# Performance work log

Hardware: AMD Instinct MI355X
Metric: run time of the kernel (lower is better)

Reference implementation:

```python
import jax, jax.numpy as jnp
from jax import lax
import numpy as np

B, T, H, W, C = 16, 64, 64, 64, 3
ACTION_DIM = 2
ENC_FEAT = 2 * 2 * 256  # conv output 2x2x256 flattened
LSTM1, LSTM2 = 512, 256
FORGET_BIAS = 1.0


def setup_inputs() -> dict:
    key = jax.random.key(0)
    ks = jax.random.split(key, 20)
    f32 = jnp.float32

    def glorot(k, shape):
        fan_in = int(np.prod(shape[:-1]))
        return jax.random.normal(k, shape, f32) * np.sqrt(2.0 / fan_in)

    inp = {
        'frames': jax.random.normal(ks[0], (B, T, H, W, C), f32),
        'actions': jax.random.normal(ks[1], (B, T, ACTION_DIM), f32),
        # conv encoder: kernel 4, stride 2, VALID, relu
        'w1': glorot(ks[2], (4, 4, 3, 32)),   'b1': jnp.zeros((32,), f32),
        'w2': glorot(ks[3], (4, 4, 32, 64)),  'b2': jnp.zeros((64,), f32),
        'w3': glorot(ks[4], (4, 4, 64, 128)), 'b3': jnp.zeros((128,), f32),
        'w4': glorot(ks[5], (4, 4, 128, 256)),'b4': jnp.zeros((256,), f32),
        # LSTM cells, TF gate order (i, j, f, o)
        'k_l1': glorot(ks[6], (ENC_FEAT + ACTION_DIM + LSTM1, 4 * LSTM1)),
        'b_l1': jnp.zeros((4 * LSTM1,), f32),
        'k_l2': glorot(ks[7], (LSTM1 + LSTM2, 4 * LSTM2)),
        'b_l2': jnp.zeros((4 * LSTM2,), f32),
        # dense head
        'w_d1': glorot(ks[8], (LSTM2, 128)), 'b_d1': jnp.zeros((128,), f32),
        'w_d2': glorot(ks[9], (128, 1)),     'b_d2': jnp.zeros((1,), f32),
    }
    return inp


def _conv(x, w, b):
    y = lax.conv_general_dilated(x, w, (2, 2), 'VALID',
                                 dimension_numbers=('NHWC', 'HWIO', 'NHWC'))
    return jax.nn.relu(y + b)


def _lstm_cell(x, h, c, k, b, hidden):
    gates = jnp.concatenate([x, h], axis=-1) @ k + b
    i, j, f, o = jnp.split(gates, 4, axis=-1)
    c_new = jax.nn.sigmoid(f + FORGET_BIAS) * c + jax.nn.sigmoid(i) * jnp.tanh(j)
    h_new = jax.nn.sigmoid(o) * jnp.tanh(c_new)
    return h_new, c_new


def reference(frames, actions, w1, b1, w2, b2, w3, b3, w4, b4,
              k_l1, b_l1, k_l2, b_l2, w_d1, b_d1, w_d2, b_d2):
    b, t = frames.shape[0], frames.shape[1]
    # CNN encoder over all frames at once
    x = frames.reshape(b * t, H, W, C)
    x = _conv(x, w1, b1)
    x = _conv(x, w2, b2)
    x = _conv(x, w3, b3)
    x = _conv(x, w4, b4)                      # [b*t, 2, 2, 256]
    enc = x.reshape(b, t, ENC_FEAT)
    lstm_in = jnp.concatenate([enc, actions], axis=-1)  # [b, t, 1026]

    # 2-layer stacked LSTM via scan over time (time-major)
    xs = jnp.swapaxes(lstm_in, 0, 1)          # [t, b, 1026]
    c1 = jnp.zeros((b, LSTM1), frames.dtype)
    h1 = jnp.zeros((b, LSTM1), frames.dtype)
    c2 = jnp.zeros((b, LSTM2), frames.dtype)
    h2 = jnp.zeros((b, LSTM2), frames.dtype)

    def step(carry, x_t):
        c1, h1, c2, h2 = carry
        h1n, c1n = _lstm_cell(x_t, h1, c1, k_l1, b_l1, LSTM1)
        h2n, c2n = _lstm_cell(h1n, h2, c2, k_l2, b_l2, LSTM2)
        return (c1n, h1n, c2n, h2n), h2n

    _, hs = lax.scan(step, (c1, h1, c2, h2), xs)  # hs: [t, b, 256]
    lstm_out = jnp.swapaxes(hs, 0, 1)              # [b, t, 256]

    d1 = jax.nn.relu(lstm_out @ w_d1 + b_d1)
    out = d1 @ w_d2 + b_d2                          # [b, t, 1]
    return out
```

## Files before the change

### kernel.cpp

```cpp
#include <hip/hip_runtime.h>

#define DI __device__ __forceinline__

DI float sigm(float x)  { return 1.0f / (1.0f + __expf(-x)); }
DI float tanh_(float x) { return 2.0f / (1.0f + __expf(-2.0f * x)) - 1.0f; }

DI float cload(const float* p) {
  return __hip_atomic_load(p, __ATOMIC_RELAXED, __HIP_MEMORY_SCOPE_AGENT);
}
DI void cstore(float* p, float v) {
  __hip_atomic_store(p, v, __ATOMIC_RELAXED, __HIP_MEMORY_SCOPE_AGENT);
}

DI void fma4(float4& a, float s, const float4& w) {
  a.x += s * w.x; a.y += s * w.y; a.z += s * w.z; a.w += s * w.w;
}
DI float4 relu4(float4 a) {
  return make_float4(fmaxf(a.x, 0.f), fmaxf(a.y, 0.f), fmaxf(a.z, 0.f), fmaxf(a.w, 0.f));
}

__global__ void conv1_k4(const float* __restrict__ in, const float* __restrict__ w,
                         const float* __restrict__ bias, float* __restrict__ out) {
  int idx = blockIdx.x * 256 + threadIdx.x;
  if (idx >= 1024 * 31 * 16 * 8) return;
  int c4 = idx & 7;  int t = idx >> 3;
  int xp = t & 15;   t >>= 4;
  int y = t % 31;    int n = t / 31;
  const float* ip = in + (((size_t)n * 64 + 2 * y) * 64 + 4 * xp) * 3;
  bool v1 = (xp < 15);
  int off1 = v1 ? 6 : 0;
  float4 bv = *(const float4*)(bias + c4 * 4);
  float4 a0 = bv, a1 = bv;
#pragma unroll
  for (int ky = 0; ky < 4; ++ky) {
#pragma unroll
    for (int kx = 0; kx < 4; ++kx) {
      const float* ipr = ip + (ky * 64 + kx) * 3;
      const float* wp  = w + ((ky * 4 + kx) * 3) * 32 + c4 * 4;
#pragma unroll
      for (int ci = 0; ci < 3; ++ci) {
        float4 wv = *(const float4*)(wp + ci * 32);
        float i0 = ipr[ci], i1 = ipr[off1 + ci];
        fma4(a0, i0, wv);
        fma4(a1, i1, wv);
      }
    }
  }
  int x0 = 2 * xp;
  float* op = out + ((size_t)n * 31 * 31 + (size_t)y * 31 + x0) * 32 + c4 * 4;
  *(float4*)op = relu4(a0);
  if (v1) *(float4*)(op + 32) = relu4(a1);
}

template <int CIN, int COUT, int NTILE, int WIN, int WOUT>
__global__ __launch_bounds__(512)
void conv_lds2(const float* __restrict__ in, const float* __restrict__ w,
               const float* __restrict__ bias, float* __restrict__ out, int ostride) {
  constexpr int K    = 16 * CIN;
  constexpr int NC4  = NTILE / 4;
  constexpr int XPB  = 512 / NC4;
  constexpr int XPI  = (WOUT / 2) * WOUT;
  constexpr int XPH  = 1024 * XPI / 2;
  __shared__ float Wl[K * NTILE];
  const int tid = threadIdx.x;
  const int cs  = blockIdx.y;
  constexpr int TOT4 = K * NC4;
  for (int i = tid; i < TOT4; i += 512) {
    int k = i / NC4, c4 = i % NC4;
    *(float4*)&Wl[k * NTILE + c4 * 4] =
        *(const float4*)&w[(size_t)k * COUT + cs * NTILE + c4 * 4];
  }
  __syncthreads();
  const int c4l  = tid % NC4;
  const int xpul = tid / NC4;
  int g0 = blockIdx.x * XPB + xpul;
  int g1 = g0 + XPH;
  int n0 = g0 / XPI, r0 = g0 % XPI;
  int y0 = r0 / (WOUT / 2), xp0 = r0 % (WOUT / 2);
  int n1 = g1 / XPI, r1 = g1 % XPI;
  int y1 = r1 / (WOUT / 2), xp1 = r1 % (WOUT / 2);
  const float* ip0 = in + (((size_t)n0 * WIN + 2 * y0) * WIN + 4 * xp0) * CIN;
  const float* ip1 = in + (((size_t)n1 * WIN + 2 * y1) * WIN + 4 * xp1) * CIN;
  float4 bv = *(const float4*)(bias + cs * NTILE + c4l * 4);
  float4 a00 = bv, a01 = bv, a10 = bv, a11 = bv;
#pragma unroll
  for (int kk = 0; kk < 16; ++kk) {
    int ky = kk >> 2, kx = kk & 3;
    const float* i0r = ip0 + (ky * WIN + kx) * CIN;
    const float* i1r = ip1 + (ky * WIN + kx) * CIN;
    const float* wpr = Wl + kk * CIN * NTILE + c4l * 4;
#pragma unroll 4
    for (int ci4 = 0; ci4 < CIN / 4; ++ci4) {
      float4 p00 = *(const float4*)(i0r + ci4 * 4);
      float4 p01 = *(const float4*)(i0r + 2 * CIN + ci4 * 4);
      float4 p10 = *(const float4*)(i1r + ci4 * 4);
      float4 p11 = *(const float4*)(i1r + 2 * CIN + ci4 * 4);
      const float* wq = wpr + (size_t)(ci4 * 4) * NTILE;
      float4 w0 = *(const float4*)(wq);
      fma4(a00, p00.x, w0); fma4(a01, p01.x, w0); fma4(a10, p10.x, w0); fma4(a11, p11.x, w0);
      float4 w1v = *(const float4*)(wq + NTILE);
      fma4(a00, p00.y, w1v); fma4(a01, p01.y, w1v); fma4(a10, p10.y, w1v); fma4(a11, p11.y, w1v);
      float4 w2v = *(const float4*)(wq + 2 * NTILE);
      fma4(a00, p00.z, w2v); fma4(a01, p01.z, w2v); fma4(a10, p10.z, w2v); fma4(a11, p11.z, w2v);
      float4 w3v = *(const float4*)(wq + 3 * NTILE);
      fma4(a00, p00.w, w3v); fma4(a01, p01.w, w3v); fma4(a10, p10.w, w3v); fma4(a11, p11.w, w3v);
    }
  }
  float* o0 = out + (size_t)n0 * ostride + ((size_t)y0 * WOUT + 2 * xp0) * COUT + cs * NTILE + c4l * 4;
  *(float4*)o0          = relu4(a00);
  *(float4*)(o0 + COUT) = relu4(a01);
  float* o1 = out + (size_t)n1 * ostride + ((size_t)y1 * WOUT + 2 * xp1) * COUT + cs * NTILE + c4l * 4;
  *(float4*)o1          = relu4(a10);
  *(float4*)(o1 + COUT) = relu4(a11);
}

__global__ void act_copy(const float* __restrict__ act, float* __restrict__ xin) {
  int i = blockIdx.x * 256 + threadIdx.x;
  if (i < 2048) xin[(size_t)(i >> 1) * 1026 + 1024 + (i & 1)] = act[i];
}

__global__ void gemm_xpart(const float* __restrict__ A, const float* __restrict__ Bw,
                           const float* __restrict__ bias, float* __restrict__ C) {
  __shared__ float As[16][64];
  __shared__ float Bs[16][64];
  const int tid = threadIdx.x;
  const int tx = tid & 15, ty = tid >> 4;
  const int m0 = blockIdx.y * 64, n0 = blockIdx.x * 64;
  float acc[4][4] = {};
  for (int k0 = 0; k0 < 1026; k0 += 16) {
#pragma unroll
    for (int i = 0; i < 4; ++i) {
      int lin = tid + i * 256;
      int ka = lin & 15, mm = lin >> 4;
      As[ka][mm] = (k0 + ka < 1026) ? A[(size_t)(m0 + mm) * 1026 + k0 + ka] : 0.0f;
      int kb = lin >> 6, nn = lin & 63;
      Bs[kb][nn] = (k0 + kb < 1026) ? Bw[(size_t)(k0 + kb) * 2048 + n0 + nn] : 0.0f;
    }
    __syncthreads();
#pragma unroll
    for (int kk = 0; kk < 16; ++kk) {
      float av[4], bv[4];
#pragma unroll
      for (int i = 0; i < 4; ++i) { av[i] = As[kk][ty * 4 + i]; bv[i] = Bs[kk][tx * 4 + i]; }
#pragma unroll
      for (int i = 0; i < 4; ++i)
#pragma unroll
        for (int j = 0; j < 4; ++j) acc[i][j] += av[i] * bv[j];
    }
    __syncthreads();
  }
#pragma unroll
  for (int i = 0; i < 4; ++i) {
    int m = m0 + ty * 4 + i;
    int xrow = (m & 63) * 16 + (m >> 6);
#pragma unroll
    for (int j = 0; j < 4; ++j) {
      int n = n0 + tx * 4 + j;
      C[(size_t)xrow * 2048 + n] = acc[i][j] + bias[n];
    }
  }
}

__global__ void __launch_bounds__(512, 1)
lstm_k(const float* __restrict__ xpart,
       const float* __restrict__ kl1,
       const float* __restrict__ kl2,
       const float* __restrict__ bl2,
       float* __restrict__ h1b, float* __restrict__ c1,
       float* __restrict__ h2b, float* __restrict__ c2,
       unsigned* __restrict__ bar,
       float* __restrict__ out_seq) {
  __shared__ float big[12544];
  __shared__ float red2[2176];
  __shared__ float gs1[544];
  __shared__ float gs2[272];
  float* stg1 = big;
  float* red1 = big + 8192;
  float* stg2 = big;
  const int tid = threadIdx.x;
  const int blk = blockIdx.x;
  const float* Wh1 = kl1 + (size_t)1026 * 2048;

  const int cA  = tid & 31, ks1 = tid >> 5;
  const int k0A = ks1 * 32;
  const int pA  = (cA & 3) * 512 + blk * 8 + (cA >> 2);
  const int cB  = tid & 15, ks2 = tid >> 4;
  const int k0B = ks2 * 24;
  const int pB  = (cB & 3) * 256 + blk * 4 + (cB >> 2);
  const int cR  = tid >> 4, bR = tid & 15;
  const int pR1 = (cR & 3) * 512 + blk * 8 + (cR >> 2);
  const int pR2 = (cR & 3) * 256 + blk * 4 + (cR >> 2);

  float w1r[32], w2r[24];
#pragma unroll
  for (int i = 0; i < 32; ++i) w1r[i] = Wh1[(size_t)(k0A + i) * 2048 + pA];
#pragma unroll
  for (int i = 0; i < 24; ++i) w2r[i] = kl2[(size_t)(k0B + i) * 1024 + pB];
  const float blv = bl2[pR2];

  for (int t = 0; t < 64; ++t) {
    const float* h1c = h1b + (size_t)(t & 1) * 8192;
    float* h1n       = h1b + (size_t)((t + 1) & 1) * 8192;
    const float* h2c = h2b + (size_t)(t & 1) * 4096;
    float* h2n       = h2b + (size_t)((t + 1) & 1) * 4096;

    float xpv = xpart[(size_t)((t << 4) + bR) * 2048 + pR1];

    float sv[16];
#pragma unroll
    for (int j = 0; j < 16; ++j) sv[j] = cload(h1c + (j << 9) + tid);
    __syncthreads();
#pragma unroll
    for (int j = 0; j < 16; ++j) stg1[(j << 9) + tid] = sv[j];
    __syncthreads();

    float acc[16];
#pragma unroll
    for (int b = 0; b < 16; ++b) acc[b] = 0.f;
#pragma unroll
    for (int bp = 0; bp < 8; ++bp) {
      const float* pa = stg1 + (bp * 2) * 512 + k0A;
      const float* pb = pa + 512;
      float4 va[8], vb[8];
#pragma unroll
      for (int i = 0; i < 8; ++i) va[i] = *(const float4*)(pa + i * 4);
#pragma unroll
      for (int i = 0; i < 8; ++i) vb[i] = *(const float4*)(pb + i * 4);
      const float* fa = (const float*)va;
      const float* fb = (const float*)vb;
#pragma unroll
      for (int j = 0; j < 32; ++j) {
        acc[bp * 2]     = fmaf(w1r[j], fa[j], acc[bp * 2]);
        acc[bp * 2 + 1] = fmaf(w1r[j], fb[j], acc[bp * 2 + 1]);
      }
    }
    {
      float fc[16];
#pragma unroll
      for (int b = 0; b < 16; ++b) fc[b] = acc[b] + __shfl_xor(acc[b], 32);
      int p = tid >> 6;
      int half = (ks1 & 1) * 8;
      float* dst = red1 + p * 544 + cA * 17 + half;
#pragma unroll
      for (int j = 0; j < 8; ++j) dst[j] = fc[half + j];
    }
    __syncthreads();
    {
      float s = xpv;
#pragma unroll
      for (int p = 0; p < 8; ++p) s += red1[p * 544 + cR * 17 + bR];
      gs1[cR * 17 + bR] = s;
    }
    __syncthreads();
    if (tid < 128) {
      int u_l = tid >> 4, b = tid & 15;
      int u = blk * 8 + u_l;
      float gi = gs1[(u_l * 4 + 0) * 17 + b];
      float gj = gs1[(u_l * 4 + 1) * 17 + b];
      float gf = gs1[(u_l * 4 + 2) * 17 + b];
      float go = gs1[(u_l * 4 + 3) * 17 + b];
      float cold = c1[b * 512 + u];
      float cn = sigm(gf + 1.0f) * cold + sigm(gi) * tanh_(gj);
      float hn = sigm(go) * tanh_(cn);
      c1[b * 512 + u] = cn;
      cstore(h1n + b * 512 + u, hn);
    }
    __syncthreads();

    if (tid == 0) {
      unsigned tgt = 8u * (t + 1);
      unsigned old = __hip_atomic_fetch_add(&bar[(blk >> 3) * 32], 1u,
                                            __ATOMIC_RELAXED, __HIP_MEMORY_SCOPE_AGENT);
      if (old == tgt - 1)
        __hip_atomic_fetch_add(&bar[256], 1u, __ATOMIC_RELAXED, __HIP_MEMORY_SCOPE_AGENT);
      while (__hip_atomic_load(&bar[256], __ATOMIC_RELAXED, __HIP_MEMORY_SCOPE_AGENT) < tgt)
        __builtin_amdgcn_s_sleep(2);
    }
    __syncthreads();

    float sw[24];
#pragma unroll
    for (int j = 0; j < 24; ++j) {
      int e = (j << 9) + tid;
      sw[j] = (j < 16) ? cload(h1n + e) : cload(h2c + (e - 8192));
    }
#pragma unroll
    for (int j = 0; j < 24; ++j) {
      if (j < 16) stg2[j * 768 + tid] = sw[j];
      else {
        int b = (j - 16) * 2 + (tid >> 8);
        stg2[b * 768 + 512 + (tid & 255)] = sw[j];
      }
    }
    __syncthreads();

#pragma unroll
    for (int b = 0; b < 16; ++b) acc[b] = 0.f;
#pragma unroll
    for (int bp = 0; bp < 8; ++bp) {
      const float* pa = stg2 + (bp * 2) * 768 + k0B;
      const float* pb = pa + 768;
      float4 va[6], vb[6];
#pragma unroll
      for (int i = 0; i < 6; ++i) va[i] = *(const float4*)(pa + i * 4);
#pragma unroll
      for (int i = 0; i < 6; ++i) vb[i] = *(const float4*)(pb + i * 4);
      const float* fa = (const float*)va;
      const float* fb = (const float*)vb;
#pragma unroll
      for (int j = 0; j < 24; ++j) {
        acc[bp * 2]     = fmaf(w2r[j], fa[j], acc[bp * 2]);
        acc[bp * 2 + 1] = fmaf(w2r[j], fb[j], acc[bp * 2 + 1]);
      }
    }
    {
      float fc[16];
#pragma unroll
      for (int b = 0; b < 16; ++b) {
        float s = acc[b] + __shfl_xor(acc[b], 16);
        fc[b] = s + __shfl_xor(s, 32);
      }
      int q = tid >> 6;
      int s4 = (ks2 & 3) * 4;
      float* dst = red2 + q * 272 + cB * 17 + s4;
#pragma unroll
      for (int j = 0; j < 4; ++j) dst[j] = fc[s4 + j];
    }
    __syncthreads();
    if (tid < 256) {
      float s = blv;
#pragma unroll
      for (int p = 0; p < 8; ++p) s += red2[p * 272 + cR * 17 + bR];
      gs2[cR * 17 + bR] = s;
    }
    __syncthreads();
    if (tid < 64) {
      int u_l = tid >> 4, b = tid & 15;
      int u = blk * 4 + u_l;
      float gi = gs2[(u_l * 4 + 0) * 17 + b];
      float gj = gs2[(u_l * 4 + 1) * 17 + b];
      float gf = gs2[(u_l * 4 + 2) * 17 + b];
      float go = gs2[(u_l * 4 + 3) * 17 + b];
      float cold = c2[b * 256 + u];
      float cn = sigm(gf + 1.0f) * cold + sigm(gi) * tanh_(gj);
      float hn = sigm(go) * tanh_(cn);
      c2[b * 256 + u] = cn;
      cstore(h2n + b * 256 + u, hn);
      out_seq[(size_t)((b << 6) + t) * 256 + u] = hn;
    }
  }
}

__global__ void head_k(const float* __restrict__ xin, const float* __restrict__ wd1,
                       const float* __restrict__ bd1, const float* __restrict__ wd2,
                       const float* __restrict__ bd2, float* __restrict__ out) {
  __shared__ float xs[4][256];
  __shared__ float ps[4][128];
  int r0 = blockIdx.x * 4;
  int tid = threadIdx.x;
  for (int i = tid; i < 1024; i += 128) xs[i >> 8][i & 255] = xin[(size_t)r0 * 256 + i];
  __syncthreads();
  float w2 = wd2[tid];
  float bb = bd1[tid];
#pragma unroll
  for (int rr = 0; rr < 4; ++rr) {
    float acc = bb;
#pragma unroll 8
    for (int k = 0; k < 256; ++k) acc += xs[rr][k] * wd1[k * 128 + tid];
    ps[rr][tid] = fmaxf(acc, 0.0f) * w2;
  }
  __syncthreads();
  if (tid < 4) {
    float s = bd2[0];
    for (int k = 0; k < 128; ++k) s += ps[tid][k];
    out[r0 + tid] = s;
  }
}

extern "C" void kernel_launch(void* const* d_in, const int* in_sizes, int n_in,
                              void* d_out, int out_size, void* d_ws, size_t ws_size,
                              hipStream_t stream) {
  const float* frames  = (const float*)d_in[0];
  const float* actions = (const float*)d_in[1];
  const float* w1 = (const float*)d_in[2];   const float* b1 = (const float*)d_in[3];
  const float* w2 = (const float*)d_in[4];   const float* b2 = (const float*)d_in[5];
  const float* w3 = (const float*)d_in[6];   const float* b3 = (const float*)d_in[7];
  const float* w4 = (const float*)d_in[8];   const float* b4 = (const float*)d_in[9];
  const float* kl1 = (const float*)d_in[10]; const float* bl1 = (const float*)d_in[11];
  const float* kl2 = (const float*)d_in[12]; const float* bl2 = (const float*)d_in[13];
  const float* wd1 = (const float*)d_in[14]; const float* bd1 = (const float*)d_in[15];
  const float* wd2 = (const float*)d_in[16]; const float* bd2 = (const float*)d_in[17];
  float* out = (float*)d_out;

  float* ws = (float*)d_ws;
  float* a1    = ws;
  float* a2    = ws + 31490048u;
  float* a3    = ws;
  float* xin   = ws + 31490048u;
  float* xpart = ws + 44335104u;
  float* h1b   = ws + 46432256u;
  float* c1    = ws + 46448640u;
  float* h2b   = ws + 46456832u;
  float* c2    = ws + 46465024u;
  unsigned* bar = (unsigned*)(ws + 46469120u);
  float* lout  = ws + 46469632u;

  hipMemsetAsync(h1b, 0, (36864 + 512) * sizeof(float), stream);

  conv1_k4<<<15872, 256, 0, stream>>>(frames, w1, b1, a1);
  conv_lds2<32, 64, 32, 31, 14><<<dim3(784, 2), 512, 0, stream>>>(a1, w2, b2, a2, 14 * 14 * 64);
  conv_lds2<64, 128, 16, 14, 6><<<dim3(72, 8), 512, 0, stream>>>(a2, w3, b3, a3, 6 * 6 * 128);
  conv_lds2<128, 256, 8, 6, 2><<<dim3(4, 32), 512, 0, stream>>>(a3, w4, b4, xin, 1026);
  act_copy<<<8, 256, 0, stream>>>(actions, xin);
  gemm_xpart<<<dim3(32, 16), 256, 0, stream>>>(xin, kl1, bl1, xpart);

  void* args[10];
  args[0] = (void*)&xpart; args[1] = (void*)&kl1; args[2] = (void*)&kl2; args[3] = (void*)&bl2;
  args[4] = (void*)&h1b;   args[5] = (void*)&c1;  args[6] = (void*)&h2b; args[7] = (void*)&c2;
  args[8] = (void*)&bar;   args[9] = (void*)&lout;
  hipLaunchCooperativeKernel((void*)lstm_k, dim3(64), dim3(512), args, 0, stream);

  head_k<<<256, 128, 0, stream>>>(lout, wd1, bd1, wd2, bd2, out);
}
```

Before: 2.773 ms.

## Split LSTM layers into pipelined block groups with per-block flags; restructure conv loop

The cooperative LSTM kernel now runs layer 1 on 64 blocks and layer 2 on 16 separate blocks. The two groups synchronise through per-block step flags instead of one global barrier, so layer 2 of step t can overlap layer 1 of step t+1. The conv kernels drop from four output pairs per thread to two, with a software-prefetched row of inputs reused across kx, and launch twice as many blocks. This adds polling traffic and heavier register use in layer-2 blocks (96 weights each), in exchange for shorter serial dependency chains and better conv load scheduling.

```diff
diff --git a/kernel.cpp b/kernel.cpp
--- a/kernel.cpp
+++ b/kernel.cpp
@@ -9,6 +9,12 @@
   return __hip_atomic_load(p, __ATOMIC_RELAXED, __HIP_MEMORY_SCOPE_AGENT);
 }
 DI void cstore(float* p, float v) {
+  __hip_atomic_store(p, v, __ATOMIC_RELAXED, __HIP_MEMORY_SCOPE_AGENT);
+}
+DI unsigned uload(const unsigned* p) {
+  return __hip_atomic_load(p, __ATOMIC_RELAXED, __HIP_MEMORY_SCOPE_AGENT);
+}
+DI void ustore(unsigned* p, unsigned v) {
   __hip_atomic_store(p, v, __ATOMIC_RELAXED, __HIP_MEMORY_SCOPE_AGENT);
 }
 
@@ -54,13 +60,14 @@
 
 template <int CIN, int COUT, int NTILE, int WIN, int WOUT>
 __global__ __launch_bounds__(512)
-void conv_lds2(const float* __restrict__ in, const float* __restrict__ w,
+void conv_lds3(const float* __restrict__ in, const float* __restrict__ w,
                const float* __restrict__ bias, float* __restrict__ out, int ostride) {
   constexpr int K    = 16 * CIN;
   constexpr int NC4  = NTILE / 4;
   constexpr int XPB  = 512 / NC4;
   constexpr int XPI  = (WOUT / 2) * WOUT;
-  constexpr int XPH  = 1024 * XPI / 2;
+  constexpr int C4N  = CIN / 4;
+  constexpr int NIT  = 4 * C4N;
   __shared__ float Wl[K * NTILE];
   const int tid = threadIdx.x;
   const int cs  = blockIdx.y;
@@ -73,45 +80,44 @@
   __syncthreads();
   const int c4l  = tid % NC4;
   const int xpul = tid / NC4;
-  int g0 = blockIdx.x * XPB + xpul;
-  int g1 = g0 + XPH;
-  int n0 = g0 / XPI, r0 = g0 % XPI;
-  int y0 = r0 / (WOUT / 2), xp0 = r0 % (WOUT / 2);
-  int n1 = g1 / XPI, r1 = g1 % XPI;
-  int y1 = r1 / (WOUT / 2), xp1 = r1 % (WOUT / 2);
-  const float* ip0 = in + (((size_t)n0 * WIN + 2 * y0) * WIN + 4 * xp0) * CIN;
-  const float* ip1 = in + (((size_t)n1 * WIN + 2 * y1) * WIN + 4 * xp1) * CIN;
+  int gxp = blockIdx.x * XPB + xpul;
+  int n = gxp / XPI, r = gxp % XPI;
+  int y = r / (WOUT / 2), xp = r % (WOUT / 2);
+  const float* ip = in + (((size_t)n * WIN + 2 * y) * WIN + 4 * xp) * CIN;
   float4 bv = *(const float4*)(bias + cs * NTILE + c4l * 4);
-  float4 a00 = bv, a01 = bv, a10 = bv, a11 = bv;
-#pragma unroll
-  for (int kk = 0; kk < 16; ++kk) {
-    int ky = kk >> 2, kx = kk & 3;
-    const float* i0r = ip0 + (ky * WIN + kx) * CIN;
-    const float* i1r = ip1 + (ky * WIN + kx) * CIN;
-    const float* wpr = Wl + kk * CIN * NTILE + c4l * 4;
-#pragma unroll 4
-    for (int ci4 = 0; ci4 < CIN / 4; ++ci4) {
-      float4 p00 = *(const float4*)(i0r + ci4 * 4);
-      float4 p01 = *(const float4*)(i0r + 2 * CIN + ci4 * 4);
-      float4 p10 = *(const float4*)(i1r + ci4 * 4);
-      float4 p11 = *(const float4*)(i1r + 2 * CIN + ci4 * 4);
-      const float* wq = wpr + (size_t)(ci4 * 4) * NTILE;
+  float4 a0 = bv, a1 = bv;
+
+  float4 cur[6], nxt[6];
+#pragma unroll
+  for (int cc = 0; cc < 6; ++cc) cur[cc] = *(const float4*)(ip + cc * CIN);
+#pragma unroll 2
+  for (int it = 0; it < NIT; ++it) {
+    int ky = it / C4N, ci4 = it % C4N;
+    if (it + 1 < NIT) {
+      int ky2 = (it + 1) / C4N, ci42 = (it + 1) % C4N;
+      const float* base = ip + (ky2 * WIN) * CIN + ci42 * 4;
+#pragma unroll
+      for (int cc = 0; cc < 6; ++cc) nxt[cc] = *(const float4*)(base + cc * CIN);
+    }
+    const float* wr = Wl + ((ky * 4) * CIN + ci4 * 4) * NTILE + c4l * 4;
+#pragma unroll
+    for (int kx = 0; kx < 4; ++kx) {
+      const float* wq = wr + (size_t)kx * CIN * NTILE;
       float4 w0 = *(const float4*)(wq);
-      fma4(a00, p00.x, w0); fma4(a01, p01.x, w0); fma4(a10, p10.x, w0); fma4(a11, p11.x, w0);
+      fma4(a0, cur[kx].x, w0);     fma4(a1, cur[kx + 2].x, w0);
       float4 w1v = *(const float4*)(wq + NTILE);
-      fma4(a00, p00.y, w1v); fma4(a01, p01.y, w1v); fma4(a10, p10.y, w1v); fma4(a11, p11.y, w1v);
+      fma4(a0, cur[kx].y, w1v);    fma4(a1, cur[kx + 2].y, w1v);
       float4 w2v = *(const float4*)(wq + 2 * NTILE);
-      fma4(a00, p00.z, w2v); fma4(a01, p01.z, w2v); fma4(a10, p10.z, w2v); fma4(a11, p11.z, w2v);
+      fma4(a0, cur[kx].z, w2v);    fma4(a1, cur[kx + 2].z, w2v);
       float4 w3v = *(const float4*)(wq + 3 * NTILE);
-      fma4(a00, p00.w, w3v); fma4(a01, p01.w, w3v); fma4(a10, p10.w, w3v); fma4(a11, p11.w, w3v);
-    }
-  }
-  float* o0 = out + (size_t)n0 * ostride + ((size_t)y0 * WOUT + 2 * xp0) * COUT + cs * NTILE + c4l * 4;
-  *(float4*)o0          = relu4(a00);
-  *(float4*)(o0 + COUT) = relu4(a01);
-  float* o1 = out + (size_t)n1 * ostride + ((size_t)y1 * WOUT + 2 * xp1) * COUT + cs * NTILE + c4l * 4;
-  *(float4*)o1          = relu4(a10);
-  *(float4*)(o1 + COUT) = relu4(a11);
+      fma4(a0, cur[kx].w, w3v);    fma4(a1, cur[kx + 2].w, w3v);
+    }
+#pragma unroll
+    for (int cc = 0; cc < 6; ++cc) cur[cc] = nxt[cc];
+  }
+  float* op = out + (size_t)n * ostride + ((size_t)y * WOUT + 2 * xp) * COUT + cs * NTILE + c4l * 4;
+  *(float4*)op          = relu4(a0);
+  *(float4*)(op + COUT) = relu4(a1);
 }
 
 __global__ void act_copy(const float* __restrict__ act, float* __restrict__ xin) {
@@ -168,185 +174,198 @@
        const float* __restrict__ bl2,
        float* __restrict__ h1b, float* __restrict__ c1,
        float* __restrict__ h2b, float* __restrict__ c2,
-       unsigned* __restrict__ bar,
+       unsigned* __restrict__ flg,
        float* __restrict__ out_seq) {
   __shared__ float big[12544];
-  __shared__ float red2[2176];
   __shared__ float gs1[544];
-  __shared__ float gs2[272];
-  float* stg1 = big;
-  float* red1 = big + 8192;
-  float* stg2 = big;
+  __shared__ float gs2[1088];
   const int tid = threadIdx.x;
   const int blk = blockIdx.x;
-  const float* Wh1 = kl1 + (size_t)1026 * 2048;
-
-  const int cA  = tid & 31, ks1 = tid >> 5;
-  const int k0A = ks1 * 32;
-  const int pA  = (cA & 3) * 512 + blk * 8 + (cA >> 2);
-  const int cB  = tid & 15, ks2 = tid >> 4;
-  const int k0B = ks2 * 24;
-  const int pB  = (cB & 3) * 256 + blk * 4 + (cB >> 2);
-  const int cR  = tid >> 4, bR = tid & 15;
-  const int pR1 = (cR & 3) * 512 + blk * 8 + (cR >> 2);
-  const int pR2 = (cR & 3) * 256 + blk * 4 + (cR >> 2);
-
-  float w1r[32], w2r[24];
-#pragma unroll
-  for (int i = 0; i < 32; ++i) w1r[i] = Wh1[(size_t)(k0A + i) * 2048 + pA];
-#pragma unroll
-  for (int i = 0; i < 24; ++i) w2r[i] = kl2[(size_t)(k0B + i) * 1024 + pB];
-  const float blv = bl2[pR2];
-
-  for (int t = 0; t < 64; ++t) {
-    const float* h1c = h1b + (size_t)(t & 1) * 8192;
-    float* h1n       = h1b + (size_t)((t + 1) & 1) * 8192;
-    const float* h2c = h2b + (size_t)(t & 1) * 4096;
-    float* h2n       = h2b + (size_t)((t + 1) & 1) * 4096;
-
-    float xpv = xpart[(size_t)((t << 4) + bR) * 2048 + pR1];
-
-    float sv[16];
-#pragma unroll
-    for (int j = 0; j < 16; ++j) sv[j] = cload(h1c + (j << 9) + tid);
-    __syncthreads();
-#pragma unroll
-    for (int j = 0; j < 16; ++j) stg1[(j << 9) + tid] = sv[j];
-    __syncthreads();
-
-    float acc[16];
-#pragma unroll
-    for (int b = 0; b < 16; ++b) acc[b] = 0.f;
-#pragma unroll
-    for (int bp = 0; bp < 8; ++bp) {
-      const float* pa = stg1 + (bp * 2) * 512 + k0A;
-      const float* pb = pa + 512;
-      float4 va[8], vb[8];
-#pragma unroll
-      for (int i = 0; i < 8; ++i) va[i] = *(const float4*)(pa + i * 4);
-#pragma unroll
-      for (int i = 0; i < 8; ++i) vb[i] = *(const float4*)(pb + i * 4);
-      const float* fa = (const float*)va;
-      const float* fb = (const float*)vb;
-#pragma unroll
-      for (int j = 0; j < 32; ++j) {
-        acc[bp * 2]     = fmaf(w1r[j], fa[j], acc[bp * 2]);
-        acc[bp * 2 + 1] = fmaf(w1r[j], fb[j], acc[bp * 2 + 1]);
-      }
-    }
-    {
-      float fc[16];
-#pragma unroll
-      for (int b = 0; b < 16; ++b) fc[b] = acc[b] + __shfl_xor(acc[b], 32);
-      int p = tid >> 6;
-      int half = (ks1 & 1) * 8;
-      float* dst = red1 + p * 544 + cA * 17 + half;
-#pragma unroll
-      for (int j = 0; j < 8; ++j) dst[j] = fc[half + j];
-    }
-    __syncthreads();
-    {
-      float s = xpv;
-#pragma unroll
-      for (int p = 0; p < 8; ++p) s += red1[p * 544 + cR * 17 + bR];
-      gs1[cR * 17 + bR] = s;
-    }
-    __syncthreads();
-    if (tid < 128) {
-      int u_l = tid >> 4, b = tid & 15;
-      int u = blk * 8 + u_l;
-      float gi = gs1[(u_l * 4 + 0) * 17 + b];
-      float gj = gs1[(u_l * 4 + 1) * 17 + b];
-      float gf = gs1[(u_l * 4 + 2) * 17 + b];
-      float go = gs1[(u_l * 4 + 3) * 17 + b];
-      float cold = c1[b * 512 + u];
-      float cn = sigm(gf + 1.0f) * cold + sigm(gi) * tanh_(gj);
-      float hn = sigm(go) * tanh_(cn);
-      c1[b * 512 + u] = cn;
-      cstore(h1n + b * 512 + u, hn);
-    }
-    __syncthreads();
-
-    if (tid == 0) {
-      unsigned tgt = 8u * (t + 1);
-      unsigned old = __hip_atomic_fetch_add(&bar[(blk >> 3) * 32], 1u,
-                                            __ATOMIC_RELAXED, __HIP_MEMORY_SCOPE_AGENT);
-      if (old == tgt - 1)
-        __hip_atomic_fetch_add(&bar[256], 1u, __ATOMIC_RELAXED, __HIP_MEMORY_SCOPE_AGENT);
-      while (__hip_atomic_load(&bar[256], __ATOMIC_RELAXED, __HIP_MEMORY_SCOPE_AGENT) < tgt)
-        __builtin_amdgcn_s_sleep(2);
-    }
-    __syncthreads();
-
-    float sw[24];
-#pragma unroll
-    for (int j = 0; j < 24; ++j) {
-      int e = (j << 9) + tid;
-      sw[j] = (j < 16) ? cload(h1n + e) : cload(h2c + (e - 8192));
-    }
-#pragma unroll
-    for (int j = 0; j < 24; ++j) {
-      if (j < 16) stg2[j * 768 + tid] = sw[j];
-      else {
-        int b = (j - 16) * 2 + (tid >> 8);
-        stg2[b * 768 + 512 + (tid & 255)] = sw[j];
-      }
-    }
-    __syncthreads();
-
-#pragma unroll
-    for (int b = 0; b < 16; ++b) acc[b] = 0.f;
-#pragma unroll
-    for (int bp = 0; bp < 8; ++bp) {
-      const float* pa = stg2 + (bp * 2) * 768 + k0B;
-      const float* pb = pa + 768;
-      float4 va[6], vb[6];
-#pragma unroll
-      for (int i = 0; i < 6; ++i) va[i] = *(const float4*)(pa + i * 4);
-#pragma unroll
-      for (int i = 0; i < 6; ++i) vb[i] = *(const float4*)(pb + i * 4);
-      const float* fa = (const float*)va;
-      const float* fb = (const float*)vb;
+  unsigned* flag1 = flg;
+  unsigned* flag2 = flg + 64;
+
+  if (blk < 64) {
+    float* stg1 = big;
+    float* red1 = big + 8192;
+    const float* Wh1 = kl1 + (size_t)1026 * 2048;
+    const int cA  = tid & 31, ks1 = tid >> 5;
+    const int k0A = ks1 * 32;
+    const int pA  = (cA & 3) * 512 + blk * 8 + (cA >> 2);
+    const int cR  = tid >> 4, bR = tid & 15;
+    const int pR1 = (cR & 3) * 512 + blk * 8 + (cR >> 2);
+    float w1r[32];
+#pragma unroll
+    for (int i = 0; i < 32; ++i) w1r[i] = Wh1[(size_t)(k0A + i) * 2048 + pA];
+
+    for (int t = 0; t < 64; ++t) {
+      const float* h1c = h1b + (size_t)(t & 1) * 8192;
+      float* h1n       = h1b + (size_t)((t + 1) & 1) * 8192;
+      float xpv = xpart[(size_t)((t << 4) + bR) * 2048 + pR1];
+
+      float sv[16];
+#pragma unroll
+      for (int j = 0; j < 16; ++j) sv[j] = cload(h1c + (j << 9) + tid);
+#pragma unroll
+      for (int j = 0; j < 16; ++j) stg1[(j << 9) + tid] = sv[j];
+      __syncthreads();
+
+      float acc[16];
+#pragma unroll
+      for (int b = 0; b < 16; ++b) acc[b] = 0.f;
+#pragma unroll
+      for (int bp = 0; bp < 8; ++bp) {
+        const float* pa = stg1 + (bp * 2) * 512 + k0A;
+        const float* pb = pa + 512;
+        float4 va[8], vb[8];
+#pragma unroll
+        for (int i = 0; i < 8; ++i) va[i] = *(const float4*)(pa + i * 4);
+#pragma unroll
+        for (int i = 0; i < 8; ++i) vb[i] = *(const float4*)(pb + i * 4);
+        const float* fa = (const float*)va;
+        const float* fb = (const float*)vb;
+#pragma unroll
+        for (int j = 0; j < 32; ++j) {
+          acc[bp * 2]     = fmaf(w1r[j], fa[j], acc[bp * 2]);
+          acc[bp * 2 + 1] = fmaf(w1r[j], fb[j], acc[bp * 2 + 1]);
+        }
+      }
+      {
+        float fc[16];
+#pragma unroll
+        for (int b = 0; b < 16; ++b) fc[b] = acc[b] + __shfl_xor(acc[b], 32);
+        int p = tid >> 6;
+        int half = (ks1 & 1) * 8;
+        float* dst = red1 + p * 544 + cA * 17 + half;
+#pragma unroll
+        for (int j = 0; j < 8; ++j) dst[j] = fc[half + j];
+      }
+      __syncthreads();
+      {
+        float s = xpv;
+#pragma unroll
+        for (int p = 0; p < 8; ++p) s += red1[p * 544 + cR * 17 + bR];
+        gs1[cR * 17 + bR] = s;
+      }
+      __syncthreads();
+      if (tid < 128) {
+        int u_l = tid >> 4, b = tid & 15;
+        int u = blk * 8 + u_l;
+        float gi = gs1[(u_l * 4 + 0) * 17 + b];
+        float gj = gs1[(u_l * 4 + 1) * 17 + b];
+        float gf = gs1[(u_l * 4 + 2) * 17 + b];
+        float go = gs1[(u_l * 4 + 3) * 17 + b];
+        float cold = c1[b * 512 + u];
+        float cn = sigm(gf + 1.0f) * cold + sigm(gi) * tanh_(gj);
+        float hn = sigm(go) * tanh_(cn);
+        c1[b * 512 + u] = cn;
+        cstore(h1n + b * 512 + u, hn);
+      }
+      __syncthreads();
+      if (tid == 0) ustore(flag1 + blk, (unsigned)(t + 1));
+      if (t < 63 && tid < 64) {
+        unsigned tgt1 = (unsigned)(t + 1), tgt2 = (unsigned)t;
+        for (;;) {
+          bool ok = uload(flag1 + tid) >= tgt1;
+          if (tid < 16) ok = ok && (uload(flag2 + tid) >= tgt2);
+          if (__all(ok)) break;
+          __builtin_amdgcn_s_sleep(1);
+        }
+      }
+      __syncthreads();
+    }
+  } else {
+    const int blk2 = blk - 64;
+    float* stg2 = big;
+    float* red  = big;
+    const int cB  = tid & 63, ks2 = tid >> 6;
+    const int k0B = ks2 * 96;
+    const int pB  = (cB & 3) * 256 + blk2 * 16 + (cB >> 2);
+    const int colR = tid & 63, bq = tid >> 6;
+    const float blvR = bl2[(colR & 3) * 256 + blk2 * 16 + (colR >> 2)];
+    float w2r[96];
+#pragma unroll
+    for (int i = 0; i < 96; ++i) w2r[i] = kl2[(size_t)(k0B + i) * 1024 + pB];
+
+    for (int s = 0; s < 64; ++s) {
+      const float* h1n = h1b + (size_t)((s + 1) & 1) * 8192;
+      const float* h2c = h2b + (size_t)(s & 1) * 4096;
+      float* h2n       = h2b + (size_t)((s + 1) & 1) * 4096;
+
+      if (tid < 64) {
+        unsigned tgt1 = (unsigned)(s + 1), tgt2 = (unsigned)s;
+        for (;;) {
+          bool ok = uload(flag1 + tid) >= tgt1;
+          if (tid < 16) ok = ok && (uload(flag2 + tid) >= tgt2);
+          if (__all(ok)) break;
+          __builtin_amdgcn_s_sleep(1);
+        }
+      }
+      __syncthreads();
+
+      float sw[24];
 #pragma unroll
       for (int j = 0; j < 24; ++j) {
-        acc[bp * 2]     = fmaf(w2r[j], fa[j], acc[bp * 2]);
-        acc[bp * 2 + 1] = fmaf(w2r[j], fb[j], acc[bp * 2 + 1]);
-      }
-    }
-    {
-      float fc[16];
+        int e = (j << 9) + tid;
+        sw[j] = (j < 16) ? cload(h1n + e) : cload(h2c + (e - 8192));
+      }
+#pragma unroll
+      for (int j = 0; j < 24; ++j) {
+        if (j < 16) stg2[j * 768 + tid] = sw[j];
+        else {
+          int e = ((j - 16) << 9) + tid;
+          stg2[(e >> 8) * 768 + 512 + (e & 255)] = sw[j];
+        }
+      }
+      __syncthreads();
+
+      float acc[16];
+#pragma unroll
+      for (int b = 0; b < 16; ++b) acc[b] = 0.f;
 #pragma unroll
       for (int b = 0; b < 16; ++b) {
-        float s = acc[b] + __shfl_xor(acc[b], 16);
-        fc[b] = s + __shfl_xor(s, 32);
-      }
-      int q = tid >> 6;
-      int s4 = (ks2 & 3) * 4;
-      float* dst = red2 + q * 272 + cB * 17 + s4;
-#pragma unroll
-      for (int j = 0; j < 4; ++j) dst[j] = fc[s4 + j];
-    }
-    __syncthreads();
-    if (tid < 256) {
-      float s = blv;
-#pragma unroll
-      for (int p = 0; p < 8; ++p) s += red2[p * 272 + cR * 17 + bR];
-      gs2[cR * 17 + bR] = s;
-    }
-    __syncthreads();
-    if (tid < 64) {
-      int u_l = tid >> 4, b = tid & 15;
-      int u = blk * 4 + u_l;
-      float gi = gs2[(u_l * 4 + 0) * 17 + b];
-      float gj = gs2[(u_l * 4 + 1) * 17 + b];
-      float gf = gs2[(u_l * 4 + 2) * 17 + b];
-      float go = gs2[(u_l * 4 + 3) * 17 + b];
-      float cold = c2[b * 256 + u];
-      float cn = sigm(gf + 1.0f) * cold + sigm(gi) * tanh_(gj);
-      float hn = sigm(go) * tanh_(cn);
-      c2[b * 256 + u] = cn;
-      cstore(h2n + b * 256 + u, hn);
-      out_seq[(size_t)((b << 6) + t) * 256 + u] = hn;
+        const float* pb_ = stg2 + b * 768 + k0B;
+#pragma unroll
+        for (int sub = 0; sub < 4; ++sub) {
+          float4 va[6];
+#pragma unroll
+          for (int i = 0; i < 6; ++i) va[i] = *(const float4*)(pb_ + sub * 24 + i * 4);
+          const float* fa = (const float*)va;
+#pragma unroll
+          for (int j = 0; j < 24; ++j)
+            acc[b] = fmaf(w2r[sub * 24 + j], fa[j], acc[b]);
+        }
+      }
+      __syncthreads();
+#pragma unroll
+      for (int j = 0; j < 16; ++j) red[ks2 * 1088 + cB * 17 + j] = acc[j];
+      __syncthreads();
+      {
+#pragma unroll
+        for (int h = 0; h < 2; ++h) {
+          int b = bq + h * 8;
+          float sum = blvR;
+#pragma unroll
+          for (int w = 0; w < 8; ++w) sum += red[w * 1088 + colR * 17 + b];
+          gs2[colR * 17 + b] = sum;
+        }
+      }
+      __syncthreads();
+      if (tid < 256) {
+        int u_l = tid >> 4, b = tid & 15;
+        int u = blk2 * 16 + u_l;
+        float gi = gs2[(u_l * 4 + 0) * 17 + b];
+        float gj = gs2[(u_l * 4 + 1) * 17 + b];
+        float gf = gs2[(u_l * 4 + 2) * 17 + b];
+        float go = gs2[(u_l * 4 + 3) * 17 + b];
+        float cold = c2[b * 256 + u];
+        float cn = sigm(gf + 1.0f) * cold + sigm(gi) * tanh_(gj);
+        float hn = sigm(go) * tanh_(cn);
+        c2[b * 256 + u] = cn;
+        cstore(h2n + b * 256 + u, hn);
+        out_seq[(size_t)((b << 6) + s) * 256 + u] = hn;
+      }
+      __syncthreads();
+      if (tid == 0) ustore(flag2 + blk2, (unsigned)(s + 1));
     }
   }
 }
@@ -402,23 +421,23 @@
   float* c1    = ws + 46448640u;
   float* h2b   = ws + 46456832u;
   float* c2    = ws + 46465024u;
-  unsigned* bar = (unsigned*)(ws + 46469120u);
+  unsigned* flg = (unsigned*)(ws + 46469120u);
   float* lout  = ws + 46469632u;
 
   hipMemsetAsync(h1b, 0, (36864 + 512) * sizeof(float), stream);
 
   conv1_k4<<<15872, 256, 0, stream>>>(frames, w1, b1, a1);
-  conv_lds2<32, 64, 32, 31, 14><<<dim3(784, 2), 512, 0, stream>>>(a1, w2, b2, a2, 14 * 14 * 64);
-  conv_lds2<64, 128, 16, 14, 6><<<dim3(72, 8), 512, 0, stream>>>(a2, w3, b3, a3, 6 * 6 * 128);
-  conv_lds2<128, 256, 8, 6, 2><<<dim3(4, 32), 512, 0, stream>>>(a3, w4, b4, xin, 1026);
+  conv_lds3<32, 64, 32, 31, 14><<<dim3(1568, 2), 512, 0, stream>>>(a1, w2, b2, a2, 14 * 14 * 64);
+  conv_lds3<64, 128, 16, 14, 6><<<dim3(144, 8), 512, 0, stream>>>(a2, w3, b3, a3, 6 * 6 * 128);
+  conv_lds3<128, 256, 8, 6, 2><<<dim3(8, 32), 512, 0, stream>>>(a3, w4, b4, xin, 1026);
   act_copy<<<8, 256, 0, stream>>>(actions, xin);
   gemm_xpart<<<dim3(32, 16), 256, 0, stream>>>(xin, kl1, bl1, xpart);
 
   void* args[10];
   args[0] = (void*)&xpart; args[1] = (void*)&kl1; args[2] = (void*)&kl2; args[3] = (void*)&bl2;
   args[4] = (void*)&h1b;   args[5] = (void*)&c1;  args[6] = (void*)&h2b; args[7] = (void*)&c2;
-  args[8] = (void*)&bar;   args[9] = (void*)&lout;
-  hipLaunchCooperativeKernel((void*)lstm_k, dim3(64), dim3(512), args, 0, stream);
+  args[8] = (void*)&flg;   args[9] = (void*)&lout;
+  hipLaunchCooperativeKernel((void*)lstm_k, dim3(80), dim3(512), args, 0, stream);
 
   head_k<<<256, 128, 0, stream>>>(lout, wd1, bd1, wd2, bd2, out);
 }
```

After: 2.601 ms. 1.07x faster.
